# Performance work log

Hardware: AMD Instinct MI355X
Metric: run time of the kernel (lower is better)

Reference implementation:

```python
import jax, jax.numpy as jnp
import numpy as np

T = 32  # simulation_length
L = 4   # number of NeuralCores in the chain


def to_uniform_spikes(x, cycle, sim_len):
    """Uniform spike encoding: emit round(x*T) spikes evenly spaced over T cycles.
    Faithful to SpikingUnifiedCoreFlow.to_uniform_spikes."""
    N = jnp.round(x * sim_len).astype(jnp.int32)
    mask = (N != 0) & (N != sim_len) & (cycle < sim_len)
    N_safe = jnp.maximum(N, 1)
    spacing = sim_len / N_safe.astype(x.dtype)          # T / N
    fire = mask & (jnp.floor(cycle / spacing) < N_safe) & (jnp.floor(jnp.mod(cycle, spacing)) == 0)
    out = fire.astype(x.dtype)
    return jnp.where(N == sim_len, jnp.ones_like(out), out)  # saturated channels fire every cycle


def setup_inputs() -> dict:
    key = jax.random.key(0)
    k0, k1 = jax.random.split(key)
    x = jax.random.uniform(k0, (128, 1024), dtype=jnp.float32)          # activations in [0,1]
    weights = jax.random.normal(k1, (L, 1024, 1024), dtype=jnp.float32) * 0.02  # (neurons, axons) per core
    thresholds = jnp.ones((L,), dtype=jnp.float32)
    return {"x": x, "weights": weights, "thresholds": thresholds}


def reference(x, weights, thresholds):
    """Rate-mode spiking simulation over a chain of NeuralCores.
    Per cycle: encode input to spikes (Uniform), propagate through cores with
    LIF integration (membrane += W @ spikes; spike = threshold < membrane;
    membrane -= spike * threshold), output = mean spike train of last core."""
    B = x.shape[0]
    H = weights.shape[1]

    def step(mem, cycle):
        sig = to_uniform_spikes(x, cycle, T)            # (B, axons_in)
        new_mems = []
        for l in range(L):
            m = mem[l] + sig @ weights[l].T             # F.linear(sig, W)
            s = (thresholds[l] < m).astype(x.dtype)     # thresholding_mode '<'
            m = m - s * thresholds[l]                   # Default firing: subtract reset
            new_mems.append(m)
            sig = s                                     # feed downstream core this cycle
        return jnp.stack(new_mems), sig                 # sig = last core spikes

    mem0 = jnp.zeros((L, B, H), dtype=x.dtype)
    _, out_spikes = jax.lax.scan(step, mem0, jnp.arange(T))  # (T, B, H)
    return out_spikes.mean(axis=0)                      # spike counts -> rates
```

## Files before the change

### kernel.cpp

```cpp
#include <hip/hip_runtime.h>
#include <stdint.h>


typedef __attribute__((ext_vector_type(4)))  int   i32x4;
typedef __attribute__((ext_vector_type(16))) int   i32x16;
typedef __attribute__((ext_vector_type(4)))  float f32x4;

#define SCALE_F 4294967296.0f
#define NSL 4

__device__ __forceinline__ void gload16(const void* g, void* l) {
    __builtin_amdgcn_global_load_lds(
        (const __attribute__((address_space(1))) void*)g,
        (__attribute__((address_space(3))) void*)l, 16, 0, 0);
}

__device__ __forceinline__ i32x4 expand16(unsigned int f) {
    i32x4 r;
    #pragma unroll
    for (int d = 0; d < 4; ++d)
        r[d] = (int)((((f >> (4 * d)) & 0xFu) * 0x00204081u) & 0x01010101u);
    return r;
}

__global__ void k_prep(const float* __restrict__ x, const float* __restrict__ w,
                       uint32_t* __restrict__ Am, signed char* __restrict__ planes) {
    if (blockIdx.x < 4096) {
        int tid = blockIdx.x * 256 + threadIdx.x;
        int l = tid >> 18;
        int rest4 = (tid & 0x3FFFF) << 2;
        f32x4 wv = *reinterpret_cast<const f32x4*>(w + ((size_t)l << 20) + rest4);
        long long q[4];
        #pragma unroll
        for (int i = 0; i < 4; ++i) q[i] = llrintf(wv[i] * SCALE_F);
        #pragma unroll
        for (int s = 0; s < NSL; ++s) {
            uint32_t pack = 0;
            #pragma unroll
            for (int i = 0; i < 4; ++i) {
                int d = (int)(signed char)((unsigned char)(q[i] & 255));
                q[i] = (q[i] - d) >> 8;
                pack |= ((uint32_t)(unsigned char)d) << (8 * i);
            }
            *reinterpret_cast<uint32_t*>(planes + (((size_t)(l * NSL + s)) << 20) + rest4) = pack;
        }
    } else {
        const int wid  = ((blockIdx.x - 4096) * 256 + threadIdx.x) >> 6;
        const int lane = threadIdx.x & 63;
        const int b = wid >> 4, kc = wid & 15;
        float v = x[b * 1024 + kc * 64 + lane];
        int N = (int)rintf(v * 32.0f);
        uint32_t bits = 0;
        if (N >= 32) {
            bits = 0xFFFFFFFFu;
        } else if (N > 0) {
            float spacing = 32.0f / (float)N;
            #pragma unroll
            for (int t = 0; t < 32; ++t) {
                float fm = fmodf((float)t, spacing);
                if (fm < 1.0f) bits |= (1u << t);
            }
        }
        uint32_t cap = 0;
        #pragma unroll
        for (int t = 0; t < 32; ++t) {
            unsigned long long bal = __ballot((bits >> t) & 1u);
            if (lane == t)      cap = (uint32_t)bal;
            if (lane == t + 32) cap = (uint32_t)(bal >> 32);
        }
        const int t = lane & 31, ww = lane >> 5;
        Am[(size_t)(b * 32 + t) * 32 + kc * 2 + ww] = cap;
    }
}

__global__ __launch_bounds__(512, 4) void k_fused(
        const uint32_t* __restrict__ Am,
        const signed char* __restrict__ planes,
        const float* __restrict__ th,
        uint32_t* __restrict__ AmNext,
        float* __restrict__ out,
        int layer) {
    __shared__ alignas(16) signed char lds[2][32768];

    const int tid  = threadIdx.x;
    const int lane = tid & 63;
    const int wave = tid >> 6;
    const int sg   = wave >> 2;
    const int mw   = (wave >> 1) & 1;
    const int nw   = wave & 1;
    const int lr   = lane & 31;
    const int hi   = lane >> 5;

    const int xc = blockIdx.x & 7, q = blockIdx.x >> 3;
    const int nTile = xc * 2 + (q & 1);
    const int mTile = q >> 1;
    const int mBase = mTile * 128, nBase = nTile * 64;

    const signed char* srcB[NSL];
    {
        const int r0 = tid >> 3, qs = tid & 7;
        const int sw0 = (qs ^ (r0 & 7)) * 16;
        #pragma unroll
        for (int s = 0; s < NSL; ++s)
            srcB[s] = planes + (((size_t)(layer * NSL + s)) << 20)
                    + (size_t)(nBase + r0) * 1024 + sw0;
    }
    const uint32_t* aRow0 = Am + (size_t)(mBase + mw * 64 + lr) * 32;
    const uint32_t* aRow1 = aRow0 + 32 * 32;

    int baddr[4];
    {
        const int brow = nw * 32 + lr;
        #pragma unroll
        for (int ks = 0; ks < 4; ++ks)
            baddr[ks] = brow * 128 + (((ks * 2 + hi) ^ (brow & 7)) * 16);
    }

    i32x16 acc[2][2];
    #pragma unroll
    for (int m = 0; m < 2; ++m)
        #pragma unroll
        for (int s = 0; s < 2; ++s)
            #pragma unroll
            for (int r = 0; r < 16; ++r) acc[m][s][r] = 0;

    auto STAGE = [&](int buf, int c) {
        const int ko = c * 128;
        gload16(srcB[0] + ko, &lds[buf][0]     + tid * 16);
        gload16(srcB[1] + ko, &lds[buf][8192]  + tid * 16);
        gload16(srcB[2] + ko, &lds[buf][16384] + tid * 16);
        gload16(srcB[3] + ko, &lds[buf][24576] + tid * 16);
    };

    i32x4 amr0[2], amr1[2];
    STAGE(0, 0);
    amr0[0] = *reinterpret_cast<const i32x4*>(aRow0);
    amr1[0] = *reinterpret_cast<const i32x4*>(aRow1);

    #pragma unroll
    for (int c = 0; c < 8; ++c) {
        const int buf = c & 1;
        const signed char* lb = &lds[buf][0];

        if (c + 1 < 8) {
            STAGE(buf ^ 1, c + 1);
            amr0[(c + 1) & 1] = *reinterpret_cast<const i32x4*>(aRow0 + (c + 1) * 4);
            amr1[(c + 1) & 1] = *reinterpret_cast<const i32x4*>(aRow1 + (c + 1) * 4);
        }

        if (c + 1 < 8) asm volatile("s_waitcnt vmcnt(6)" ::: "memory");
        else           asm volatile("s_waitcnt vmcnt(0)" ::: "memory");
        __builtin_amdgcn_s_barrier();
        asm volatile("" ::: "memory");

        __builtin_amdgcn_s_setprio(1);
        #pragma unroll
        for (int ks = 0; ks < 4; ++ks) {
            i32x4 af0 = expand16((((unsigned)amr0[c & 1][ks]) >> (16 * hi)) & 0xFFFFu);
            i32x4 af1 = expand16((((unsigned)amr1[c & 1][ks]) >> (16 * hi)) & 0xFFFFu);
            #pragma unroll
            for (int s = 0; s < 2; ++s) {
                i32x4 bf = *reinterpret_cast<const i32x4*>(
                        lb + (sg * 2 + s) * 8192 + baddr[ks]);
                acc[0][s] = __builtin_amdgcn_mfma_i32_32x32x32_i8(af0, bf, acc[0][s], 0, 0, 0);
                acc[1][s] = __builtin_amdgcn_mfma_i32_32x32x32_i8(af1, bf, acc[1][s], 0, 0, 0);
            }
        }
        __builtin_amdgcn_s_setprio(0);

        __builtin_amdgcn_s_barrier();
        asm volatile("" ::: "memory");
    }

    long long pKeep[16], pSend[16];
    #pragma unroll
    for (int r = 0; r < 16; ++r) {
        long long v0 = (long long)acc[0][0][r] + ((long long)acc[0][1][r] << 8);
        long long v1 = (long long)acc[1][0][r] + ((long long)acc[1][1][r] << 8);
        pKeep[r] = sg ? v1 : v0;
        pSend[r] = sg ? v0 : v1;
    }

    signed char* ex = &lds[0][0];
    const int pr = (mw * 2 + nw);
    const int reg_w = (pr * 2 + sg) * 8192;
    const int reg_r = (pr * 2 + (sg ^ 1)) * 8192;
    #pragma unroll
    for (int u = 0; u < 8; ++u) {
        i32x4 wv;
        long long a = pSend[2 * u], b = pSend[2 * u + 1];
        wv[0] = (int)a; wv[1] = (int)(a >> 32);
        wv[2] = (int)b; wv[3] = (int)(b >> 32);
        *reinterpret_cast<i32x4*>(ex + reg_w + lane * 128 + ((u ^ (lane & 7)) * 16)) = wv;
    }
    __syncthreads();
    long long tot[16];
    #pragma unroll
    for (int u = 0; u < 8; ++u) {
        i32x4 v = *reinterpret_cast<const i32x4*>(
                ex + reg_r + lane * 128 + ((u ^ (lane & 7)) * 16));
        long long a = ((long long)v[1] << 32) | (uint32_t)v[0];
        long long b = ((long long)v[3] << 32) | (uint32_t)v[2];
        tot[2 * u]     = sg ? (pKeep[2 * u]     << 16) + a : pKeep[2 * u]     + (a << 16);
        tot[2 * u + 1] = sg ? (pKeep[2 * u + 1] << 16) + b : pKeep[2 * u + 1] + (b << 16);
    }

    const long long TH = llrintf(th[layer] * SCALE_F);
    const int batch = mTile * 4 + mw * 2 + sg;
    uint32_t bits = 0;
    long long mmem = 0;
    #pragma unroll
    for (int half = 0; half < 2; ++half) {
        long long own_[8], par[8];
        #pragma unroll
        for (int r = 0; r < 8; ++r) own_[r] = tot[half * 8 + r];
        #pragma unroll
        for (int r = 0; r < 8; ++r) {
            int plo = __shfl((int)(uint32_t)own_[r], lane ^ 32, 64);
            int phi = __shfl((int)(own_[r] >> 32), lane ^ 32, 64);
            par[r] = ((long long)phi << 32) | (uint32_t)plo;
        }
        #pragma unroll
        for (int tq = 0; tq < 16; ++tq) {
            const int idx = (tq >> 3) * 4 + (tq & 3);
            const int usePar = ((tq >> 2) & 1) ^ hi;
            long long v = usePar ? par[idx] : own_[idx];
            mmem += v;
            if (mmem > TH) { mmem -= TH; bits |= (1u << (half * 16 + tq)); }
        }
    }

    if (AmNext) {
        uint32_t cap = 0;
        #pragma unroll
        for (int t = 0; t < 32; ++t) {
            unsigned long long bal = __ballot((bits >> t) & 1u);
            if (lane == t) cap = (uint32_t)bal;
        }
        if (hi == 0)
            AmNext[(size_t)(batch * 32 + lr) * 32 + nTile * 2 + nw] = cap;
    } else if (hi == 0) {
        out[batch * 1024 + nBase + nw * 32 + lr] = (float)__popc(bits) * 0.03125f;
    }
}

extern "C" void kernel_launch(void* const* d_in, const int* in_sizes, int n_in,
                              void* d_out, int out_size, void* d_ws, size_t ws_size,
                              hipStream_t stream) {
    const float* x  = (const float*)d_in[0];
    const float* w  = (const float*)d_in[1];
    const float* th = (const float*)d_in[2];
    float* out = (float*)d_out;
    char* ws = (char*)d_ws;

    signed char* planes = (signed char*)(ws);
    uint32_t*    Am0    = (uint32_t*)(ws + 16777216);
    uint32_t*    Am1    = (uint32_t*)(ws + 17301504);

    k_prep<<<4608, 256, 0, stream>>>(x, w, Am0, planes);

    uint32_t* Ain = Am0;
    uint32_t* Anx = Am1;
    for (int l = 0; l < 4; ++l) {
        k_fused<<<512, 512, 0, stream>>>(Ain, planes, th,
                                         (l < 3) ? Anx : nullptr,
                                         (l == 3) ? out : nullptr, l);
        uint32_t* tmp = Ain; Ain = Anx; Anx = tmp;
    }
}
```

Measured before the change: 114.5 us.

## Split K-chunk staging into two half-plane phases with finer-grained waits

The per-chunk load of four weight bit-planes is split into two halves, each issued after its own barrier. MFMAs on the first plane pair start once those planes have landed, while the second pair is still in flight. The aim is to overlap global-to-LDS loads with matrix compute at finer granularity than one wait per chunk. Barrier count per chunk stays at two, but the wait counts and buffer-reuse ordering become more delicate.

```diff
diff --git a/kernel.cpp b/kernel.cpp
--- a/kernel.cpp
+++ b/kernel.cpp
@@ -115,6 +115,8 @@
         for (int ks = 0; ks < 4; ++ks)
             baddr[ks] = brow * 128 + (((ks * 2 + hi) ^ (brow & 7)) * 16);
     }
+    const int sb1 = sg * 16384;
+    const int sb2 = sb1 + 8192;
 
     i32x16 acc[2][2];
     #pragma unroll
@@ -124,52 +126,66 @@
             #pragma unroll
             for (int r = 0; r < 16; ++r) acc[m][s][r] = 0;
 
-    auto STAGE = [&](int buf, int c) {
+    auto H0 = [&](int buf, int c) {
         const int ko = c * 128;
         gload16(srcB[0] + ko, &lds[buf][0]     + tid * 16);
+        gload16(srcB[2] + ko, &lds[buf][16384] + tid * 16);
+    };
+    auto H1 = [&](int buf, int c) {
+        const int ko = c * 128;
         gload16(srcB[1] + ko, &lds[buf][8192]  + tid * 16);
-        gload16(srcB[2] + ko, &lds[buf][16384] + tid * 16);
         gload16(srcB[3] + ko, &lds[buf][24576] + tid * 16);
     };
 
     i32x4 amr0[2], amr1[2];
-    STAGE(0, 0);
+    H0(0, 0);
     amr0[0] = *reinterpret_cast<const i32x4*>(aRow0);
     amr1[0] = *reinterpret_cast<const i32x4*>(aRow1);
+    H1(0, 0);
 
     #pragma unroll
     for (int c = 0; c < 8; ++c) {
         const int buf = c & 1;
         const signed char* lb = &lds[buf][0];
 
+        asm volatile("s_waitcnt vmcnt(2)" ::: "memory");
+        __builtin_amdgcn_s_barrier();
+        asm volatile("" ::: "memory");
+
         if (c + 1 < 8) {
-            STAGE(buf ^ 1, c + 1);
+            H0(buf ^ 1, c + 1);
             amr0[(c + 1) & 1] = *reinterpret_cast<const i32x4*>(aRow0 + (c + 1) * 4);
             amr1[(c + 1) & 1] = *reinterpret_cast<const i32x4*>(aRow1 + (c + 1) * 4);
         }
 
-        if (c + 1 < 8) asm volatile("s_waitcnt vmcnt(6)" ::: "memory");
+        __builtin_amdgcn_s_setprio(1);
+        #pragma unroll
+        for (int ks = 0; ks < 4; ++ks) {
+            i32x4 af0 = expand16((((unsigned)amr0[c & 1][ks]) >> (16 * hi)) & 0xFFFFu);
+            i32x4 af1 = expand16((((unsigned)amr1[c & 1][ks]) >> (16 * hi)) & 0xFFFFu);
+            i32x4 bf = *reinterpret_cast<const i32x4*>(lb + sb1 + baddr[ks]);
+            acc[0][0] = __builtin_amdgcn_mfma_i32_32x32x32_i8(af0, bf, acc[0][0], 0, 0, 0);
+            acc[1][0] = __builtin_amdgcn_mfma_i32_32x32x32_i8(af1, bf, acc[1][0], 0, 0, 0);
+        }
+        __builtin_amdgcn_s_setprio(0);
+
+        if (c + 1 < 8) asm volatile("s_waitcnt vmcnt(4)" ::: "memory");
         else           asm volatile("s_waitcnt vmcnt(0)" ::: "memory");
         __builtin_amdgcn_s_barrier();
         asm volatile("" ::: "memory");
 
+        if (c + 1 < 8) H1(buf ^ 1, c + 1);
+
         __builtin_amdgcn_s_setprio(1);
         #pragma unroll
         for (int ks = 0; ks < 4; ++ks) {
             i32x4 af0 = expand16((((unsigned)amr0[c & 1][ks]) >> (16 * hi)) & 0xFFFFu);
             i32x4 af1 = expand16((((unsigned)amr1[c & 1][ks]) >> (16 * hi)) & 0xFFFFu);
-            #pragma unroll
-            for (int s = 0; s < 2; ++s) {
-                i32x4 bf = *reinterpret_cast<const i32x4*>(
-                        lb + (sg * 2 + s) * 8192 + baddr[ks]);
-                acc[0][s] = __builtin_amdgcn_mfma_i32_32x32x32_i8(af0, bf, acc[0][s], 0, 0, 0);
-                acc[1][s] = __builtin_amdgcn_mfma_i32_32x32x32_i8(af1, bf, acc[1][s], 0, 0, 0);
-            }
+            i32x4 bf = *reinterpret_cast<const i32x4*>(lb + sb2 + baddr[ks]);
+            acc[0][1] = __builtin_amdgcn_mfma_i32_32x32x32_i8(af0, bf, acc[0][1], 0, 0, 0);
+            acc[1][1] = __builtin_amdgcn_mfma_i32_32x32x32_i8(af1, bf, acc[1][1], 0, 0, 0);
         }
         __builtin_amdgcn_s_setprio(0);
-
-        __builtin_amdgcn_s_barrier();
-        asm volatile("" ::: "memory");
     }
 
     long long pKeep[16], pSend[16];
```

After: 127.9 us. +11.8%, slower.
